# Kernel optimization log

Hardware: AMD Instinct MI355X
Metric: run time of the kernel (lower is better)

## Reference

```python
import jax, jax.numpy as jnp
import numpy as np

P = 16  # pooled samples per RoI (init kwarg)


def setup_inputs() -> dict:
    key = jax.random.key(0)
    k1, k2, k3 = jax.random.split(key, 3)
    B, T, D, K = 16, 4096, 512, 64
    feat = jax.random.normal(k1, (B, T, D), dtype=jnp.float32)
    spans = jax.random.randint(k2, (B, K, 2), 0, T)          # start/end indices
    lengths = jax.random.randint(k3, (B,), 512, T + 1)        # valid length per batch
    return {"feat": feat, "spans": spans, "lengths": lengths}


def reference(feat, spans, lengths):
    # feat: [B, T, D], spans: [B, K, 2] int, lengths: [B] int -> [B, K, P, D]
    B, T, D = feat.shape
    Lm1 = (lengths - 1)[:, None, None]                         # [B,1,1]
    sb = jnp.clip(spans, 0, Lm1)                               # clamp to [0, L-1]
    s = jnp.min(sb, axis=-1)                                   # [B,K] (swap if e < s)
    e = jnp.max(sb, axis=-1)                                   # [B,K]
    seglen = e - s + 1                                         # [B,K] segment length
    # linspace(0, seglen-1, P) per RoI, vectorized
    t = jnp.arange(P, dtype=feat.dtype) / (P - 1)              # [P] in [0,1]
    idx = t * (seglen - 1)[..., None].astype(feat.dtype)       # [B,K,P]
    idx0 = jnp.minimum(jnp.floor(idx).astype(jnp.int32),
                       (seglen - 1)[..., None].astype(jnp.int32))
    idx1 = jnp.minimum(idx0 + 1, (seglen - 1)[..., None].astype(jnp.int32))
    w = (idx - idx0.astype(feat.dtype))[..., None]             # [B,K,P,1]
    g0 = s[..., None].astype(jnp.int32) + idx0                 # [B,K,P] absolute idx
    g1 = s[..., None].astype(jnp.int32) + idx1
    gather = jax.vmap(lambda f, i: f[i])                       # per-batch gather
    f0 = gather(feat, g0)                                      # [B,K,P,D]
    f1 = gather(feat, g1)
    return (1.0 - w) * f0 + w * f1
```

## Files before the change

kernel.cpp:

```cpp
#include <hip/hip_runtime.h>


constexpr int B = 16;
constexpr int T = 4096;
constexpr int D = 512;
constexpr int K = 64;
constexpr int P = 16;

__global__ __launch_bounds__(128) void roialign1d_kernel(
    const float* __restrict__ feat,
    const int* __restrict__ spans,
    const int* __restrict__ lengths,
    float* __restrict__ out) {

    const int bkp = blockIdx.x;
    const int p   = bkp & (P - 1);
    const int bk  = bkp >> 4;
    const int b   = bk >> 6;

    const int Lm1 = lengths[b] - 1;
    int s0 = spans[bk * 2 + 0];
    int s1 = spans[bk * 2 + 1];
    s0 = min(max(s0, 0), Lm1);
    s1 = min(max(s1, 0), Lm1);
    const int s      = min(s0, s1);
    const int e      = max(s0, s1);
    const int seglen = e - s + 1;

    const float t   = (float)p / 15.0f;
    const float idx = t * (float)(seglen - 1);
    const int idx0  = min((int)floorf(idx), seglen - 1);
    const int idx1  = min(idx0 + 1, seglen - 1);
    const float w   = idx - (float)idx0;

    const float4* __restrict__ f0 =
        (const float4*)(feat + ((size_t)b * T + (size_t)(s + idx0)) * D);
    const float4* __restrict__ f1 =
        (const float4*)(feat + ((size_t)b * T + (size_t)(s + idx1)) * D);
    float4* __restrict__ o = (float4*)(out + ((size_t)bk * P + p) * D);

    const int d = threadIdx.x;
    const float4 a = f0[d];
    const float4 c = f1[d];
    float4 r;
    const float wm = 1.0f - w;
    r.x = wm * a.x + w * c.x;
    r.y = wm * a.y + w * c.y;
    r.z = wm * a.z + w * c.z;
    r.w = wm * a.w + w * c.w;
    o[d] = r;
}

extern "C" void kernel_launch(void* const* d_in, const int* in_sizes, int n_in,
                              void* d_out, int out_size, void* d_ws, size_t ws_size,
                              hipStream_t stream) {
    const float* feat    = (const float*)d_in[0];
    const int*   spans   = (const int*)d_in[1];
    const int*   lengths = (const int*)d_in[2];
    float*       out     = (float*)d_out;

    const int n_rows = B * K * P;
    roialign1d_kernel<<<n_rows, 128, 0, stream>>>(feat, spans, lengths, out);
}
```

Baseline: 182.9 us.

## Process one RoI per block with 256 threads looping over samples

Launches one block per RoI (B*K blocks of 256 threads) instead of one 128-thread block per pooled sample. Each half of the block handles alternating samples in an unrolled loop, so the span/length setup is done once per RoI and the many tiny blocks become fewer, larger ones. The cost is fewer blocks in flight (1024), which may reduce memory-level parallelism for this bandwidth-bound gather.

Result: no change. 183.7 us (+0.4%).

```diff
diff --git a/kernel.cpp b/kernel.cpp
--- a/kernel.cpp
+++ b/kernel.cpp
@@ -7,16 +7,14 @@
 constexpr int K = 64;
 constexpr int P = 16;
 
-__global__ __launch_bounds__(128) void roialign1d_kernel(
+__global__ __launch_bounds__(256) void roialign1d_kernel(
     const float* __restrict__ feat,
     const int* __restrict__ spans,
     const int* __restrict__ lengths,
     float* __restrict__ out) {
 
-    const int bkp = blockIdx.x;
-    const int p   = bkp & (P - 1);
-    const int bk  = bkp >> 4;
-    const int b   = bk >> 6;
+    const int bk = blockIdx.x;
+    const int b  = bk >> 6;
 
     const int Lm1 = lengths[b] - 1;
     int s0 = spans[bk * 2 + 0];
@@ -26,29 +24,35 @@
     const int s      = min(s0, s1);
     const int e      = max(s0, s1);
     const int seglen = e - s + 1;
+    const float segm1f = (float)(seglen - 1);
+    const int   segm1i = seglen - 1;
 
-    const float t   = (float)p / 15.0f;
-    const float idx = t * (float)(seglen - 1);
-    const int idx0  = min((int)floorf(idx), seglen - 1);
-    const int idx1  = min(idx0 + 1, seglen - 1);
-    const float w   = idx - (float)idx0;
+    const int d  = threadIdx.x & 127;
+    const int ph = threadIdx.x >> 7;
 
-    const float4* __restrict__ f0 =
-        (const float4*)(feat + ((size_t)b * T + (size_t)(s + idx0)) * D);
-    const float4* __restrict__ f1 =
-        (const float4*)(feat + ((size_t)b * T + (size_t)(s + idx1)) * D);
-    float4* __restrict__ o = (float4*)(out + ((size_t)bk * P + p) * D);
+    const float4* __restrict__ fb = (const float4*)(feat + (size_t)b * T * D);
+    float4* __restrict__ ob = (float4*)(out + (size_t)bk * P * D);
 
-    const int d = threadIdx.x;
-    const float4 a = f0[d];
-    const float4 c = f1[d];
-    float4 r;
-    const float wm = 1.0f - w;
-    r.x = wm * a.x + w * c.x;
-    r.y = wm * a.y + w * c.y;
-    r.z = wm * a.z + w * c.z;
-    r.w = wm * a.w + w * c.w;
-    o[d] = r;
+    #pragma unroll
+    for (int pp = 0; pp < P; pp += 2) {
+        const int p = pp + ph;
+
+        const float t   = (float)p / 15.0f;
+        const float idx = t * segm1f;
+        const int idx0  = min((int)floorf(idx), segm1i);
+        const int idx1  = min(idx0 + 1, segm1i);
+        const float w   = idx - (float)idx0;
+        const float wm  = 1.0f - w;
+
+        const float4 a = fb[(size_t)(s + idx0) * 128 + d];
+        const float4 c = fb[(size_t)(s + idx1) * 128 + d];
+        float4 r;
+        r.x = wm * a.x + w * c.x;
+        r.y = wm * a.y + w * c.y;
+        r.z = wm * a.z + w * c.z;
+        r.w = wm * a.w + w * c.w;
+        ob[p * 128 + d] = r;
+    }
 }
 
 extern "C" void kernel_launch(void* const* d_in, const int* in_sizes, int n_in,
@@ -59,6 +63,5 @@
     const int*   lengths = (const int*)d_in[2];
     float*       out     = (float*)d_out;
 
-    const int n_rows = B * K * P;
-    roialign1d_kernel<<<n_rows, 128, 0, stream>>>(feat, spans, lengths, out);
+    roialign1d_kernel<<<B * K, 256, 0, stream>>>(feat, spans, lengths, out);
 }
```
